# Performance work log

Hardware: AMD Instinct MI355X
Metric: run time of the kernel (lower is better)

Reference implementation:

```python
import jax, jax.numpy as jnp
import numpy as np
import math

D = 1024
H = 16
DH = D // H
FF = 4096
B, S = 2, 2048


def _layernorm(x, g, b, eps=1e-5):
    mu = jnp.mean(x, axis=-1, keepdims=True)
    var = jnp.var(x, axis=-1, keepdims=True)
    return (x - mu) * jax.lax.rsqrt(var + eps) * g + b


def _gelu_tanh(x):
    # 0.5*x*(1+tanh(sqrt(2/pi)*(x+0.044715*x^3)))
    c = math.sqrt(2.0 / math.pi)
    return 0.5 * x * (1.0 + jnp.tanh(c * (x + 0.044715 * x ** 3)))


def setup_inputs() -> dict:
    key = jax.random.key(0)
    ks = jax.random.split(key, 8)
    s = 0.02
    return {
        "x": jax.random.normal(ks[0], (B, S, D), dtype=jnp.float32),
        "ln1_g": jnp.ones((D,), jnp.float32),
        "ln1_b": jnp.zeros((D,), jnp.float32),
        "Wqkv": jax.random.normal(ks[1], (D, 3 * D), jnp.float32) * s,
        "bqkv": jnp.zeros((3 * D,), jnp.float32),
        "Wo": jax.random.normal(ks[2], (D, D), jnp.float32) * s,
        "bo": jnp.zeros((D,), jnp.float32),
        "ln2_g": jnp.ones((D,), jnp.float32),
        "ln2_b": jnp.zeros((D,), jnp.float32),
        "W1": jax.random.normal(ks[3], (D, FF), jnp.float32) * s,
        "b1": jnp.zeros((FF,), jnp.float32),
        "W2": jax.random.normal(ks[4], (FF, D), jnp.float32) * s,
        "b2": jnp.zeros((D,), jnp.float32),
    }


def reference(x, ln1_g, ln1_b, Wqkv, bqkv, Wo, bo, ln2_g, ln2_b, W1, b1, W2, b2):
    b, s, d = x.shape
    h = _layernorm(x, ln1_g, ln1_b)
    qkv = h @ Wqkv + bqkv                       # [B,S,3D]
    q, k, v = jnp.split(qkv, 3, axis=-1)
    q = q.reshape(b, s, H, DH).transpose(0, 2, 1, 3)   # [B,H,S,Dh]
    k = k.reshape(b, s, H, DH).transpose(0, 2, 1, 3)
    v = v.reshape(b, s, H, DH).transpose(0, 2, 1, 3)
    scores = jnp.einsum("bhqd,bhkd->bhqk", q, k) / math.sqrt(DH)
    probs = jax.nn.softmax(scores, axis=-1)
    attn = jnp.einsum("bhqk,bhkd->bhqd", probs, v)     # [B,H,S,Dh]
    attn = attn.transpose(0, 2, 1, 3).reshape(b, s, d)
    attn = attn @ Wo + bo
    x = x + attn
    m = _layernorm(x, ln2_g, ln2_b)
    m = _gelu_tanh(m @ W1 + b1) @ W2 + b2
    return x + m
```

## Files before the change

### kernel.cpp

```cpp
#include <hip/hip_runtime.h>
#include <hip/hip_bf16.h>
#include <cstdint>

#define D_ 1024
#define H_ 16
#define DH_ 64
#define FF_ 4096
#define B_ 2
#define S_ 2048
#define MR_ (B_ * S_)
#define BHS_ (B_ * H_ * S_)

typedef __bf16 bf16x8 __attribute__((ext_vector_type(8)));
typedef __bf16 bf16x4 __attribute__((ext_vector_type(4)));
typedef float f32x4 __attribute__((ext_vector_type(4)));
typedef float f32x16 __attribute__((ext_vector_type(16)));

__device__ __forceinline__ void g2lds16(const void* g, void* l) {
  __builtin_amdgcn_global_load_lds(
      (__attribute__((address_space(1))) void*)(uintptr_t)g,
      (__attribute__((address_space(3))) void*)(uint32_t)(uintptr_t)l,
      16, 0, 0);
}

__device__ __forceinline__ unsigned pkbf16(float lo, float hi) {
  unsigned r;
  asm("v_cvt_pk_bf16_f32 %0, %1, %2" : "=v"(r) : "v"(lo), "v"(hi));
  return r;
}

__device__ __forceinline__ float max3f(float a, float b, float c) {
  float d;
  asm("v_max3_f32 %0, %1, %2, %3" : "=v"(d) : "v"(a), "v"(b), "v"(c));
  return d;
}

__device__ __forceinline__ float rmax16(const f32x16& v) {
  float t0 = max3f(v[0], v[1], v[2]);
  float t1 = max3f(v[3], v[4], v[5]);
  float t2 = max3f(v[6], v[7], v[8]);
  float t3 = max3f(v[9], v[10], v[11]);
  float t4 = max3f(v[12], v[13], v[14]);
  return fmaxf(max3f(t0, t1, t2), max3f(t3, t4, v[15]));
}

__global__ __launch_bounds__(256) void transpose_cvt(
    const float* __restrict__ W, __hip_bfloat16* __restrict__ Wt, int K, int N) {
  __shared__ float t[32][33];
  int bx = blockIdx.x * 32;
  int by = blockIdx.y * 32;
  int tx = threadIdx.x, ty = threadIdx.y;
#pragma unroll
  for (int i = 0; i < 4; ++i)
    t[ty + 8 * i][tx] = W[(size_t)(by + ty + 8 * i) * N + bx + tx];
  __syncthreads();
#pragma unroll
  for (int i = 0; i < 4; ++i)
    Wt[(size_t)(bx + ty + 8 * i) * K + by + tx] = __float2bfloat16(t[tx][ty + 8 * i]);
}

__global__ __launch_bounds__(256) void transpose_v(
    const __hip_bfloat16* __restrict__ qkv, __hip_bfloat16* __restrict__ vT) {
  __shared__ __hip_bfloat16 t[32][33];
  int bh = blockIdx.z, b = bh >> 4, h = bh & 15;
  int s0 = blockIdx.x * 32, d0 = blockIdx.y * 32;
  int tx = threadIdx.x, ty = threadIdx.y;
#pragma unroll
  for (int i = 0; i < 4; ++i)
    t[ty + 8 * i][tx] =
        qkv[(size_t)(b * S_ + s0 + ty + 8 * i) * (3 * D_) + 2 * D_ + h * DH_ + d0 + tx];
  __syncthreads();
#pragma unroll
  for (int i = 0; i < 4; ++i)
    vT[(size_t)(bh * DH_ + d0 + ty + 8 * i) * S_ + s0 + tx] = t[tx][ty + 8 * i];
}

__global__ __launch_bounds__(256) void ln_kernel(
    const float* __restrict__ x, const float* __restrict__ g,
    const float* __restrict__ b, __hip_bfloat16* __restrict__ out) {
  int row = blockIdx.x;
  const float4* xr = (const float4*)(x + (size_t)row * D_);
  float4 v = xr[threadIdx.x];
  float s = v.x + v.y + v.z + v.w;
  float ss = v.x * v.x + v.y * v.y + v.z * v.z + v.w * v.w;
#pragma unroll
  for (int m = 1; m < 64; m <<= 1) {
    s += __shfl_xor(s, m);
    ss += __shfl_xor(ss, m);
  }
  __shared__ float rs[4], rss[4];
  int wave = threadIdx.x >> 6, lane = threadIdx.x & 63;
  if (lane == 0) { rs[wave] = s; rss[wave] = ss; }
  __syncthreads();
  s = rs[0] + rs[1] + rs[2] + rs[3];
  ss = rss[0] + rss[1] + rss[2] + rss[3];
  float mean = s * (1.0f / D_);
  float var = ss * (1.0f / D_) - mean * mean;
  float inv = rsqrtf(var + 1e-5f);
  int c = threadIdx.x * 4;
  float4 gv = ((const float4*)g)[threadIdx.x];
  float4 bv = ((const float4*)b)[threadIdx.x];
  __hip_bfloat16* o = out + (size_t)row * D_ + c;
  o[0] = __float2bfloat16((v.x - mean) * inv * gv.x + bv.x);
  o[1] = __float2bfloat16((v.y - mean) * inv * gv.y + bv.y);
  o[2] = __float2bfloat16((v.z - mean) * inv * gv.z + bv.z);
  o[3] = __float2bfloat16((v.w - mean) * inv * gv.w + bv.w);
}

template <int EPI>
__global__ __launch_bounds__(256) void gemm4(
    const __hip_bfloat16* __restrict__ A, const __hip_bfloat16* __restrict__ Bt,
    const float* __restrict__ bias, const float* __restrict__ resid,
    void* __restrict__ outp, int M, int N, int K) {
  constexpr int BM = 128, BN = 128, MF = 4, NF = 4;
  __shared__ alignas(16) __hip_bfloat16 sA[2][BM * 64];
  __shared__ alignas(16) __hip_bfloat16 sB[2][BN * 64];
  const int tid = threadIdx.x;
  const int lane = tid & 63, wave = tid >> 6;
  const int l15 = lane & 15, l4 = lane >> 4;
  const int wr = wave >> 1, wc = wave & 1;
  const int csw = (l15 & 7) << 3;

  const int gx = gridDim.x;
  int nwg = gx * gridDim.y;
  int flat = blockIdx.y * gx + blockIdx.x;
  int cpx = nwg >> 3;
  int swz = (flat & 7) * cpx + (flat >> 3);
  const int m0 = (swz / gx) * BM, n0 = (swz % gx) * BN;

  f32x4 z = {0.f, 0.f, 0.f, 0.f};
  f32x4 acc[MF][NF];
#pragma unroll
  for (int i = 0; i < MF; ++i)
#pragma unroll
    for (int j = 0; j < NF; ++j) acc[i][j] = z;

  auto stage = [&](int bu, int kt) {
#pragma unroll
    for (int it = 0; it < 4; ++it) {
      int idx = it * 256 + tid;
      int r = idx >> 3, c = (idx & 7) * 8;
      int cs = c ^ ((r & 7) << 3);
      g2lds16(A + (size_t)(m0 + r) * K + kt + cs, (void*)(&sA[bu][idx * 8]));
      g2lds16(Bt + (size_t)(n0 + r) * K + kt + cs, (void*)(&sB[bu][idx * 8]));
    }
  };

  const int nk = K / 64;
  stage(0, 0);
  asm volatile("s_waitcnt vmcnt(0)" ::: "memory");
  __builtin_amdgcn_s_barrier();

  for (int j = 0; j < nk; ++j) {
    const int cur = j & 1;
    if (j + 1 < nk) stage(cur ^ 1, (j + 1) * 64);

    __builtin_amdgcn_s_setprio(1);
#pragma unroll
    for (int kk = 0; kk < 2; ++kk) {
      int col = (kk * 32 + l4 * 8) ^ csw;
      bf16x8 bfr[NF];
#pragma unroll
      for (int nf = 0; nf < NF; ++nf)
        bfr[nf] = *(const bf16x8*)(&sB[cur][(wc * 64 + nf * 16 + l15) * 64 + col]);
#pragma unroll
      for (int mf = 0; mf < MF; ++mf) {
        bf16x8 af = *(const bf16x8*)(&sA[cur][(wr * 64 + mf * 16 + l15) * 64 + col]);
#pragma unroll
        for (int nf = 0; nf < NF; ++nf)
          acc[mf][nf] =
              __builtin_amdgcn_mfma_f32_16x16x32_bf16(af, bfr[nf], acc[mf][nf], 0, 0, 0);
      }
    }
    __builtin_amdgcn_s_setprio(0);

    asm volatile("s_waitcnt lgkmcnt(0)" ::: "memory");
    __builtin_amdgcn_sched_barrier(0);
    asm volatile("s_waitcnt vmcnt(0)" ::: "memory");
    __builtin_amdgcn_s_barrier();
    asm volatile("" ::: "memory");
  }

#pragma unroll
  for (int mf = 0; mf < MF; ++mf) {
#pragma unroll
    for (int nf = 0; nf < NF; ++nf) {
      int col = n0 + wc * 64 + nf * 16 + l15;
      float bv = bias[col];
#pragma unroll
      for (int j = 0; j < 4; ++j) {
        int row = m0 + wr * 64 + mf * 16 + l4 * 4 + j;
        size_t o = (size_t)row * N + col;
        float v = acc[mf][nf][j] + bv;
        if (EPI == 0) {
          ((__hip_bfloat16*)outp)[o] = __float2bfloat16(v);
        } else if (EPI == 1) {
          ((float*)outp)[o] = v + resid[o];
        } else {
          float a = 0.7978845608028654f * (v + 0.044715f * v * v * v);
          a = fminf(fmaxf(a, -15.f), 15.f);
          float e = __expf(2.f * a);
          float th = (e - 1.f) / (e + 1.f);
          ((__hip_bfloat16*)outp)[o] = __float2bfloat16(0.5f * v * (1.f + th));
        }
      }
    }
  }
}

template <int EPI>
__global__ __launch_bounds__(512) void gemmr3(
    const __hip_bfloat16* __restrict__ A, const __hip_bfloat16* __restrict__ Bt,
    const float* __restrict__ bias, const float* __restrict__ resid,
    void* __restrict__ outp, int M, int N, int K) {
  constexpr int BM = 128, BN = 128, MF = 4, NF = 2, WN = 4;
  __shared__ alignas(16) __hip_bfloat16 sA[3][BM * 64];
  __shared__ alignas(16) __hip_bfloat16 sB[3][BN * 64];
  const int tid = threadIdx.x;
  const int lane = tid & 63, wave = tid >> 6;
  const int l15 = lane & 15, l4 = lane >> 4;
  const int wr = wave / WN, wc = wave % WN;
  const int csw = (l15 & 7) << 3;

  const int gx = gridDim.x;
  int nwg = gx * gridDim.y;
  int flat = blockIdx.y * gx + blockIdx.x;
  int cpx = nwg >> 3;
  int swz = (flat & 7) * cpx + (flat >> 3);
  const int m0 = (swz / gx) * BM, n0 = (swz % gx) * BN;

  f32x4 z = {0.f, 0.f, 0.f, 0.f};
  f32x4 acc[MF][NF];
#pragma unroll
  for (int i = 0; i < MF; ++i)
#pragma unroll
    for (int j = 0; j < NF; ++j) acc[i][j] = z;

  auto stage = [&](int bu, int kt) {
#pragma unroll
    for (int it = 0; it < 2; ++it) {
      int idx = it * 512 + tid;
      int r = idx >> 3, c = (idx & 7) * 8;
      int cs = c ^ ((r & 7) << 3);
      g2lds16(A + (size_t)(m0 + r) * K + kt + cs, (void*)(&sA[bu][idx * 8]));
      g2lds16(Bt + (size_t)(n0 + r) * K + kt + cs, (void*)(&sB[bu][idx * 8]));
    }
  };

  const int nk = K / 64;
  stage(0, 0);
  stage(1, 64);
  asm volatile("s_waitcnt vmcnt(4)" ::: "memory");
  __builtin_amdgcn_s_barrier();

  int bu = 0, bu2 = 2;
  for (int j = 0; j < nk; ++j) {
    const bool pf = (j + 2) < nk;
    if (pf) stage(bu2, (j + 2) * 64);

    __builtin_amdgcn_s_setprio(1);
#pragma unroll
    for (int kk = 0; kk < 2; ++kk) {
      int col = (kk * 32 + l4 * 8) ^ csw;
      bf16x8 bfr[NF];
#pragma unroll
      for (int nf = 0; nf < NF; ++nf)
        bfr[nf] = *(const bf16x8*)(&sB[bu][(wc * NF * 16 + nf * 16 + l15) * 64 + col]);
#pragma unroll
      for (int mf = 0; mf < MF; ++mf) {
        bf16x8 af = *(const bf16x8*)(&sA[bu][(wr * MF * 16 + mf * 16 + l15) * 64 + col]);
#pragma unroll
        for (int nf = 0; nf < NF; ++nf)
          acc[mf][nf] =
              __builtin_amdgcn_mfma_f32_16x16x32_bf16(af, bfr[nf], acc[mf][nf], 0, 0, 0);
      }
    }
    __builtin_amdgcn_s_setprio(0);

    asm volatile("s_waitcnt lgkmcnt(0)" ::: "memory");
    __builtin_amdgcn_sched_barrier(0);
    if (pf)
      asm volatile("s_waitcnt vmcnt(4)" ::: "memory");
    else
      asm volatile("s_waitcnt vmcnt(0)" ::: "memory");
    __builtin_amdgcn_s_barrier();
    asm volatile("" ::: "memory");
    bu = (bu == 2) ? 0 : bu + 1;
    bu2 = (bu2 == 2) ? 0 : bu2 + 1;
  }

#pragma unroll
  for (int mf = 0; mf < MF; ++mf) {
#pragma unroll
    for (int nf = 0; nf < NF; ++nf) {
      int col = n0 + wc * NF * 16 + nf * 16 + l15;
      float bv = bias[col];
#pragma unroll
      for (int j = 0; j < 4; ++j) {
        int row = m0 + wr * MF * 16 + mf * 16 + l4 * 4 + j;
        size_t o = (size_t)row * N + col;
        float v = acc[mf][nf][j] + bv;
        if (EPI == 0) {
          ((__hip_bfloat16*)outp)[o] = __float2bfloat16(v);
        } else if (EPI == 1) {
          ((float*)outp)[o] = v + resid[o];
        } else {
          float a = 0.7978845608028654f * (v + 0.044715f * v * v * v);
          a = fminf(fmaxf(a, -15.f), 15.f);
          float e = __expf(2.f * a);
          float th = (e - 1.f) / (e + 1.f);
          ((__hip_bfloat16*)outp)[o] = __float2bfloat16(0.5f * v * (1.f + th));
        }
      }
    }
  }
}

__global__ __launch_bounds__(256) void attn_kernel(
    const __hip_bfloat16* __restrict__ qkv, const __hip_bfloat16* __restrict__ vT,
    __hip_bfloat16* __restrict__ opart, float* __restrict__ Mb, float* __restrict__ Lb) {
  __shared__ alignas(16) __hip_bfloat16 sK[2][64 * 64];
  __shared__ alignas(16) __hip_bfloat16 sV[2][64 * 64];
  __shared__ float sBr[4][32];
  const int tid = threadIdx.x, lane = tid & 63, wave = tid >> 6;
  const int l31 = lane & 31, hi = lane >> 5;
  const int bh = blockIdx.y, b = bh >> 4, h = bh & 15;
  const int q0 = blockIdx.x * 128;
  const int kvh = blockIdx.z;
  const int rsw = (l31 & 7) << 3;
  const float k2 = 0.125f * 1.44269504f;

  bf16x8 qf[4];
  {
    int qr = q0 + wave * 32 + l31;
    const size_t qbase = ((size_t)(b * S_ + qr)) * (3 * D_) + h * DH_;
#pragma unroll
    for (int ks = 0; ks < 4; ++ks) {
      bf16x8 q = *(const bf16x8*)(qkv + qbase + ks * 16 + hi * 8);
#pragma unroll
      for (int i = 0; i < 8; ++i) q[i] = (__bf16)((float)q[i] * k2);
      qf[ks] = q;
    }
  }

  bf16x8 onesb;
#pragma unroll
  for (int i = 0; i < 8; ++i) onesb[i] = (__bf16)1.0f;

  f32x16 acc0, acc1, accL;
#pragma unroll
  for (int r = 0; r < 16; ++r) { acc0[r] = 0.f; acc1[r] = 0.f; accL[r] = 0.f; }
  float mrun = -1e30f;

  const __hip_bfloat16* kg = qkv + (size_t)b * S_ * (3 * D_) + D_ + h * DH_;
  const __hip_bfloat16* vg = vT + (size_t)bh * DH_ * S_;

  auto stage = [&](int bu, int kv0) {
#pragma unroll
    for (int it = 0; it < 2; ++it) {
      int idx = it * 256 + tid;
      int r = idx >> 3;
      int c = (idx & 7) * 8;
      int cs = c ^ ((r & 7) << 3);
      g2lds16(kg + (size_t)(kv0 + r) * (3 * D_) + cs, (void*)(&sK[bu][idx * 8]));
      g2lds16(vg + (size_t)r * S_ + kv0 + cs, (void*)(&sV[bu][idx * 8]));
    }
  };

  const int NT = S_ / 128;
  const int t0 = kvh * NT;
  stage(0, t0 * 64);

  for (int t = 0; t < NT; ++t) {
    const int cur = t & 1;
    __syncthreads();
    if (t + 1 < NT) stage(cur ^ 1, (t0 + t + 1) * 64);

    f32x16 sf0, sf1;
#pragma unroll
    for (int r = 0; r < 16; ++r) { sf0[r] = 0.f; sf1[r] = 0.f; }
    __builtin_amdgcn_s_setprio(1);
#pragma unroll
    for (int ks = 0; ks < 4; ++ks) {
      int colsw = (ks * 16 + hi * 8) ^ rsw;
      bf16x8 kf0 = *(const bf16x8*)(&sK[cur][l31 * 64 + colsw]);
      bf16x8 kf1 = *(const bf16x8*)(&sK[cur][(32 + l31) * 64 + colsw]);
      sf0 = __builtin_amdgcn_mfma_f32_32x32x16_bf16(kf0, qf[ks], sf0, 0, 0, 0);
      sf1 = __builtin_amdgcn_mfma_f32_32x32x16_bf16(kf1, qf[ks], sf1, 0, 0, 0);
    }
    __builtin_amdgcn_s_setprio(0);

    float pm = fmaxf(rmax16(sf0), rmax16(sf1));
    if (!__all(pm - mrun <= 8.0f)) {
      float mf = fmaxf(pm, __shfl_xor(pm, 32));
      float mn = fmaxf(mrun, mf);
      float corrl = exp2f(mrun - mn);
      mrun = mn;
      sBr[wave][l31] = corrl;
#pragma unroll
      for (int r = 0; r < 16; ++r) {
        float cr = sBr[wave][(r & 3) + 8 * (r >> 2) + 4 * hi];
        acc0[r] *= cr;
        acc1[r] *= cr;
        accL[r] *= cr;
      }
    }

    bf16x8 pa[4];
#pragma unroll
    for (int kb = 0; kb < 2; ++kb) {
      const f32x16 s16 = kb ? sf1 : sf0;
#pragma unroll
      for (int ksb = 0; ksb < 2; ++ksb) {
        float p0 = exp2f(s16[8 * ksb + 0] - mrun);
        float p1 = exp2f(s16[8 * ksb + 1] - mrun);
        float p2 = exp2f(s16[8 * ksb + 2] - mrun);
        float p3 = exp2f(s16[8 * ksb + 3] - mrun);
        float p4 = exp2f(s16[8 * ksb + 4] - mrun);
        float p5 = exp2f(s16[8 * ksb + 5] - mrun);
        float p6 = exp2f(s16[8 * ksb + 6] - mrun);
        float p7 = exp2f(s16[8 * ksb + 7] - mrun);
        unsigned wa = pkbf16(p0, p1), wb = pkbf16(p2, p3);
        unsigned wc = pkbf16(p4, p5), wd = pkbf16(p6, p7);
        auto r1 = __builtin_amdgcn_permlane32_swap(wa, wc, false, false);
        auto r2 = __builtin_amdgcn_permlane32_swap(wb, wd, false, false);
        union { unsigned u[4]; bf16x8 v; } w;
        w.u[0] = r1[0]; w.u[1] = r2[0]; w.u[2] = r1[1]; w.u[3] = r2[1];
        pa[kb * 2 + ksb] = w.v;
      }
    }

    __builtin_amdgcn_s_setprio(1);
#pragma unroll
    for (int ksg = 0; ksg < 4; ++ksg) {
      int colsw = (ksg * 16 + hi * 8) ^ rsw;
      bf16x8 vf0 = *(const bf16x8*)(&sV[cur][l31 * 64 + colsw]);
      bf16x8 vf1 = *(const bf16x8*)(&sV[cur][(32 + l31) * 64 + colsw]);
      acc0 = __builtin_amdgcn_mfma_f32_32x32x16_bf16(pa[ksg], vf0, acc0, 0, 0, 0);
      acc1 = __builtin_amdgcn_mfma_f32_32x32x16_bf16(pa[ksg], vf1, acc1, 0, 0, 0);
      accL = __builtin_amdgcn_mfma_f32_32x32x16_bf16(pa[ksg], onesb, accL, 0, 0, 0);
    }
    __builtin_amdgcn_s_setprio(0);
  }

  __hip_bfloat16* op = opart + (size_t)kvh * MR_ * D_;
  float* Mp = Mb + (size_t)kvh * BHS_ + (size_t)bh * S_;
  float* Lp = Lb + (size_t)kvh * BHS_ + (size_t)bh * S_;
#pragma unroll
  for (int r = 0; r < 16; ++r) {
    int qrow = (r & 3) + 8 * (r >> 2) + 4 * hi;
    size_t obase = ((size_t)(b * S_ + q0 + wave * 32 + qrow)) * D_ + h * DH_ + l31;
    op[obase] = __float2bfloat16(acc0[r]);
    op[obase + 32] = __float2bfloat16(acc1[r]);
    if (l31 == 0) Lp[q0 + wave * 32 + qrow] = accL[r];
  }
  if (hi == 0) Mp[q0 + wave * 32 + l31] = mrun;
}

__global__ __launch_bounds__(256) void attn_combine(
    const __hip_bfloat16* __restrict__ op, const float* __restrict__ Mb,
    const float* __restrict__ Lb, __hip_bfloat16* __restrict__ out) {
  size_t base = ((size_t)blockIdx.x * 256 + threadIdx.x) * 4;
  int d = (int)(base & (D_ - 1));
  int srow = (int)(base >> 10);
  int h = d >> 6;
  int b = srow >> 11;
  int s = srow & (S_ - 1);
  size_t ml = (size_t)(b * H_ + h) * S_ + s;
  float m0 = Mb[ml], m1 = Mb[ml + BHS_];
  float l0 = Lb[ml], l1 = Lb[ml + BHS_];
  float m = fmaxf(m0, m1);
  float w0 = exp2f(m0 - m), w1 = exp2f(m1 - m);
  float invl = 1.0f / (l0 * w0 + l1 * w1);
  bf16x4 o0 = *(const bf16x4*)(op + base);
  bf16x4 o1 = *(const bf16x4*)(op + base + (size_t)MR_ * D_);
  bf16x4 ov;
#pragma unroll
  for (int j = 0; j < 4; ++j)
    ov[j] = (__bf16)(((float)o0[j] * w0 + (float)o1[j] * w1) * invl);
  *(bf16x4*)(out + base) = ov;
}

extern "C" void kernel_launch(void* const* d_in, const int* in_sizes, int n_in,
                              void* d_out, int out_size, void* d_ws, size_t ws_size,
                              hipStream_t stream) {
  const float* x = (const float*)d_in[0];
  const float* ln1_g = (const float*)d_in[1];
  const float* ln1_b = (const float*)d_in[2];
  const float* Wqkv = (const float*)d_in[3];
  const float* bqkv = (const float*)d_in[4];
  const float* Wo = (const float*)d_in[5];
  const float* bo = (const float*)d_in[6];
  const float* ln2_g = (const float*)d_in[7];
  const float* ln2_b = (const float*)d_in[8];
  const float* W1 = (const float*)d_in[9];
  const float* b1 = (const float*)d_in[10];
  const float* W2 = (const float*)d_in[11];
  const float* b2 = (const float*)d_in[12];
  float* out = (float*)d_out;

  char* ws = (char*)d_ws;
  size_t off = 0;
  auto alloc = [&](size_t bytes) {
    void* p = ws + off;
    off += (bytes + 255) & ~(size_t)255;
    return p;
  };
  __hip_bfloat16* WqkvT = (__hip_bfloat16*)alloc((size_t)3 * D_ * D_ * 2);
  __hip_bfloat16* WoT = (__hip_bfloat16*)alloc((size_t)D_ * D_ * 2);
  __hip_bfloat16* W1T = (__hip_bfloat16*)alloc((size_t)FF_ * D_ * 2);
  __hip_bfloat16* W2T = (__hip_bfloat16*)alloc((size_t)D_ * FF_ * 2);
  __hip_bfloat16* h = (__hip_bfloat16*)alloc((size_t)MR_ * D_ * 2);
  __hip_bfloat16* qkv = (__hip_bfloat16*)alloc((size_t)MR_ * FF_ * 2);
  __hip_bfloat16* ff = qkv;
  __hip_bfloat16* vT = (__hip_bfloat16*)alloc((size_t)B_ * H_ * DH_ * S_ * 2);
  __hip_bfloat16* attn_out = (__hip_bfloat16*)alloc((size_t)MR_ * D_ * 2);
  __hip_bfloat16* opart = (__hip_bfloat16*)alloc((size_t)2 * MR_ * D_ * 2);
  float* Mb = (float*)alloc((size_t)2 * BHS_ * 4);
  float* Lb = (float*)alloc((size_t)2 * BHS_ * 4);

  dim3 tb(32, 8);
  transpose_cvt<<<dim3(3 * D_ / 32, D_ / 32), tb, 0, stream>>>(Wqkv, WqkvT, D_, 3 * D_);
  transpose_cvt<<<dim3(D_ / 32, D_ / 32), tb, 0, stream>>>(Wo, WoT, D_, D_);
  transpose_cvt<<<dim3(FF_ / 32, D_ / 32), tb, 0, stream>>>(W1, W1T, D_, FF_);
  transpose_cvt<<<dim3(D_ / 32, FF_ / 32), tb, 0, stream>>>(W2, W2T, FF_, D_);
  ln_kernel<<<MR_, 256, 0, stream>>>(x, ln1_g, ln1_b, h);
  gemm4<0><<<dim3(3 * D_ / 128, MR_ / 128), 256, 0, stream>>>(
      h, WqkvT, bqkv, nullptr, qkv, MR_, 3 * D_, D_);
  transpose_v<<<dim3(S_ / 32, DH_ / 32, B_ * H_), tb, 0, stream>>>(qkv, vT);
  attn_kernel<<<dim3(S_ / 128, B_ * H_, 2), 256, 0, stream>>>(qkv, vT, opart, Mb, Lb);
  attn_combine<<<dim3(MR_ * D_ / 1024), 256, 0, stream>>>(opart, Mb, Lb, attn_out);
  gemmr3<1><<<dim3(D_ / 128, MR_ / 128), 512, 0, stream>>>(
      attn_out, WoT, bo, x, out, MR_, D_, D_);
  ln_kernel<<<MR_, 256, 0, stream>>>(out, ln2_g, ln2_b, h);
  gemm4<2><<<dim3(FF_ / 128, MR_ / 128), 256, 0, stream>>>(
      h, W1T, b1, nullptr, ff, MR_, FF_, D_);
  gemmr3<1><<<dim3(D_ / 128, MR_ / 128), 512, 0, stream>>>(
      ff, W2T, b2, out, out, MR_, D_, FF_);
}
```

Before: 240.0 us.

## Drop split-KV attention and combine kernel; use native exp2 intrinsic

Each attention block now walks the whole KV sequence and normalises its output directly by the running row sum, rather than splitting KV into two halves that a separate combine kernel merges. This removes one launch and the write and read of the partial outputs and their max/sum buffers. The cost is half as many attention blocks (512), which may leave CUs underused on a large GPU and lengthens each block's serial loop. It also swaps exp2f for the raw hardware exp2 builtin to skip range handling.

Result: faster. 221.0 us (-7.9%).

```diff
diff --git a/kernel.cpp b/kernel.cpp
--- a/kernel.cpp
+++ b/kernel.cpp
@@ -9,7 +9,6 @@
 #define B_ 2
 #define S_ 2048
 #define MR_ (B_ * S_)
-#define BHS_ (B_ * H_ * S_)
 
 typedef __bf16 bf16x8 __attribute__((ext_vector_type(8)));
 typedef __bf16 bf16x4 __attribute__((ext_vector_type(4)));
@@ -27,6 +26,10 @@
   unsigned r;
   asm("v_cvt_pk_bf16_f32 %0, %1, %2" : "=v"(r) : "v"(lo), "v"(hi));
   return r;
+}
+
+__device__ __forceinline__ float fexp2(float x) {
+  return __builtin_amdgcn_exp2f(x);
 }
 
 __device__ __forceinline__ float max3f(float a, float b, float c) {
@@ -318,7 +321,7 @@
 
 __global__ __launch_bounds__(256) void attn_kernel(
     const __hip_bfloat16* __restrict__ qkv, const __hip_bfloat16* __restrict__ vT,
-    __hip_bfloat16* __restrict__ opart, float* __restrict__ Mb, float* __restrict__ Lb) {
+    __hip_bfloat16* __restrict__ out) {
   __shared__ alignas(16) __hip_bfloat16 sK[2][64 * 64];
   __shared__ alignas(16) __hip_bfloat16 sV[2][64 * 64];
   __shared__ float sBr[4][32];
@@ -326,7 +329,6 @@
   const int l31 = lane & 31, hi = lane >> 5;
   const int bh = blockIdx.y, b = bh >> 4, h = bh & 15;
   const int q0 = blockIdx.x * 128;
-  const int kvh = blockIdx.z;
   const int rsw = (l31 & 7) << 3;
   const float k2 = 0.125f * 1.44269504f;
 
@@ -367,14 +369,13 @@
     }
   };
 
-  const int NT = S_ / 128;
-  const int t0 = kvh * NT;
-  stage(0, t0 * 64);
+  stage(0, 0);
+  const int NT = S_ / 64;
 
   for (int t = 0; t < NT; ++t) {
     const int cur = t & 1;
     __syncthreads();
-    if (t + 1 < NT) stage(cur ^ 1, (t0 + t + 1) * 64);
+    if (t + 1 < NT) stage(cur ^ 1, (t + 1) * 64);
 
     f32x16 sf0, sf1;
 #pragma unroll
@@ -394,7 +395,7 @@
     if (!__all(pm - mrun <= 8.0f)) {
       float mf = fmaxf(pm, __shfl_xor(pm, 32));
       float mn = fmaxf(mrun, mf);
-      float corrl = exp2f(mrun - mn);
+      float corrl = fexp2(mrun - mn);
       mrun = mn;
       sBr[wave][l31] = corrl;
 #pragma unroll
@@ -412,14 +413,14 @@
       const f32x16 s16 = kb ? sf1 : sf0;
 #pragma unroll
       for (int ksb = 0; ksb < 2; ++ksb) {
-        float p0 = exp2f(s16[8 * ksb + 0] - mrun);
-        float p1 = exp2f(s16[8 * ksb + 1] - mrun);
-        float p2 = exp2f(s16[8 * ksb + 2] - mrun);
-        float p3 = exp2f(s16[8 * ksb + 3] - mrun);
-        float p4 = exp2f(s16[8 * ksb + 4] - mrun);
-        float p5 = exp2f(s16[8 * ksb + 5] - mrun);
-        float p6 = exp2f(s16[8 * ksb + 6] - mrun);
-        float p7 = exp2f(s16[8 * ksb + 7] - mrun);
+        float p0 = fexp2(s16[8 * ksb + 0] - mrun);
+        float p1 = fexp2(s16[8 * ksb + 1] - mrun);
+        float p2 = fexp2(s16[8 * ksb + 2] - mrun);
+        float p3 = fexp2(s16[8 * ksb + 3] - mrun);
+        float p4 = fexp2(s16[8 * ksb + 4] - mrun);
+        float p5 = fexp2(s16[8 * ksb + 5] - mrun);
+        float p6 = fexp2(s16[8 * ksb + 6] - mrun);
+        float p7 = fexp2(s16[8 * ksb + 7] - mrun);
         unsigned wa = pkbf16(p0, p1), wb = pkbf16(p2, p3);
         unsigned wc = pkbf16(p4, p5), wd = pkbf16(p6, p7);
         auto r1 = __builtin_amdgcn_permlane32_swap(wa, wc, false, false);
@@ -443,42 +444,14 @@
     __builtin_amdgcn_s_setprio(0);
   }
 
-  __hip_bfloat16* op = opart + (size_t)kvh * MR_ * D_;
-  float* Mp = Mb + (size_t)kvh * BHS_ + (size_t)bh * S_;
-  float* Lp = Lb + (size_t)kvh * BHS_ + (size_t)bh * S_;
 #pragma unroll
   for (int r = 0; r < 16; ++r) {
     int qrow = (r & 3) + 8 * (r >> 2) + 4 * hi;
+    float ir = 1.0f / accL[r];
     size_t obase = ((size_t)(b * S_ + q0 + wave * 32 + qrow)) * D_ + h * DH_ + l31;
-    op[obase] = __float2bfloat16(acc0[r]);
-    op[obase + 32] = __float2bfloat16(acc1[r]);
-    if (l31 == 0) Lp[q0 + wave * 32 + qrow] = accL[r];
-  }
-  if (hi == 0) Mp[q0 + wave * 32 + l31] = mrun;
-}
-
-__global__ __launch_bounds__(256) void attn_combine(
-    const __hip_bfloat16* __restrict__ op, const float* __restrict__ Mb,
-    const float* __restrict__ Lb, __hip_bfloat16* __restrict__ out) {
-  size_t base = ((size_t)blockIdx.x * 256 + threadIdx.x) * 4;
-  int d = (int)(base & (D_ - 1));
-  int srow = (int)(base >> 10);
-  int h = d >> 6;
-  int b = srow >> 11;
-  int s = srow & (S_ - 1);
-  size_t ml = (size_t)(b * H_ + h) * S_ + s;
-  float m0 = Mb[ml], m1 = Mb[ml + BHS_];
-  float l0 = Lb[ml], l1 = Lb[ml + BHS_];
-  float m = fmaxf(m0, m1);
-  float w0 = exp2f(m0 - m), w1 = exp2f(m1 - m);
-  float invl = 1.0f / (l0 * w0 + l1 * w1);
-  bf16x4 o0 = *(const bf16x4*)(op + base);
-  bf16x4 o1 = *(const bf16x4*)(op + base + (size_t)MR_ * D_);
-  bf16x4 ov;
-#pragma unroll
-  for (int j = 0; j < 4; ++j)
-    ov[j] = (__bf16)(((float)o0[j] * w0 + (float)o1[j] * w1) * invl);
-  *(bf16x4*)(out + base) = ov;
+    out[obase] = __float2bfloat16(acc0[r] * ir);
+    out[obase + 32] = __float2bfloat16(acc1[r] * ir);
+  }
 }
 
 extern "C" void kernel_launch(void* const* d_in, const int* in_sizes, int n_in,
@@ -515,9 +488,6 @@
   __hip_bfloat16* ff = qkv;
   __hip_bfloat16* vT = (__hip_bfloat16*)alloc((size_t)B_ * H_ * DH_ * S_ * 2);
   __hip_bfloat16* attn_out = (__hip_bfloat16*)alloc((size_t)MR_ * D_ * 2);
-  __hip_bfloat16* opart = (__hip_bfloat16*)alloc((size_t)2 * MR_ * D_ * 2);
-  float* Mb = (float*)alloc((size_t)2 * BHS_ * 4);
-  float* Lb = (float*)alloc((size_t)2 * BHS_ * 4);
 
   dim3 tb(32, 8);
   transpose_cvt<<<dim3(3 * D_ / 32, D_ / 32), tb, 0, stream>>>(Wqkv, WqkvT, D_, 3 * D_);
@@ -528,8 +498,7 @@
   gemm4<0><<<dim3(3 * D_ / 128, MR_ / 128), 256, 0, stream>>>(
       h, WqkvT, bqkv, nullptr, qkv, MR_, 3 * D_, D_);
   transpose_v<<<dim3(S_ / 32, DH_ / 32, B_ * H_), tb, 0, stream>>>(qkv, vT);
-  attn_kernel<<<dim3(S_ / 128, B_ * H_, 2), 256, 0, stream>>>(qkv, vT, opart, Mb, Lb);
-  attn_combine<<<dim3(MR_ * D_ / 1024), 256, 0, stream>>>(opart, Mb, Lb, attn_out);
+  attn_kernel<<<dim3(S_ / 128, B_ * H_), 256, 0, stream>>>(qkv, vT, attn_out);
   gemmr3<1><<<dim3(D_ / 128, MR_ / 128), 512, 0, stream>>>(
       attn_out, WoT, bo, x, out, MR_, D_, D_);
   ln_kernel<<<MR_, 256, 0, stream>>>(out, ln2_g, ln2_b, h);
```
